# Kernel tuning notes

Hardware: AMD Instinct MI355X
Metric: run time of the kernel (lower is better)

## Reference

```python
import jax, jax.numpy as jnp
import numpy as np

B, S, D, F, E = 8, 2048, 768, 3072, 8


def setup_inputs() -> dict:
    key = jax.random.key(0)
    k1, k2, k3, k4 = jax.random.split(key, 4)
    return {
        "hidden_states": jax.random.normal(k1, (B, S, D), dtype=jnp.float32),
        "router_w": jax.random.normal(k2, (D, E), dtype=jnp.float32) * 0.02,
        "w_in": jax.random.normal(k3, (E, D, F), dtype=jnp.float32) * 0.02,
        "w_out": jax.random.normal(k4, (E, F, D), dtype=jnp.float32) * 0.02,
    }


def reference(hidden_states, router_w, w_in, w_out):
    b, s, d = hidden_states.shape
    x = hidden_states.reshape(-1, d)                    # [T, D] tokens
    router_logits = x @ router_w                        # [T, E]
    router_probs_full = jax.nn.softmax(router_logits, axis=-1)
    expert_index = jnp.argmax(router_probs_full, axis=-1)          # top-1 routing
    onehot = jax.nn.one_hot(expert_index, E, dtype=x.dtype)        # [T, E] router_mask
    top_prob = jnp.max(router_probs_full, axis=-1, keepdims=True)  # [T, 1] router_probs

    # Per-expert FFN (relu MLP); every token is processed by exactly one expert,
    # expert outputs overwrite the token (gather/scatter combine in the original).
    y = jnp.zeros_like(x)
    for e in range(E):  # fixed small expert count; weights structurally distinct
        h = jax.nn.relu(x @ w_in[e]) @ w_out[e]
        y = y + onehot[:, e:e + 1] * h

    out = (top_prob * y).reshape(b, s, d)
    return out, router_logits, expert_index
```

## Files before the change

kernel.cpp:

```cpp
#include <hip/hip_runtime.h>
#include <hip/hip_bf16.h>

constexpr int T  = 16384;
constexpr int Dh = 768;
constexpr int Fh = 3072;
constexpr int Eh = 8;
constexpr int MAXT2 = T / 256 + Eh;

typedef unsigned short ushort_t;
typedef __attribute__((ext_vector_type(8))) short  bf16x8;
typedef __attribute__((ext_vector_type(4))) float  f32x4;

static __device__ __forceinline__ ushort_t f2bf(float f) {
    unsigned u = __builtin_bit_cast(unsigned, f);
    u += 0x7FFFu + ((u >> 16) & 1u);
    return (ushort_t)(u >> 16);
}

__global__ void init_counts(int* counts) {
    if (threadIdx.x < Eh) counts[threadIdx.x] = 0;
}

__global__ __launch_bounds__(1024) void router_kernel(
    const float* __restrict__ x, const float* __restrict__ rw,
    float* __restrict__ logits_out, float* __restrict__ eidx_out,
    float* __restrict__ topp, int* __restrict__ counts, int* __restrict__ perm) {

    __shared__ float rwT[Eh][Dh];
    __shared__ int   sAmax[16];
    __shared__ int   sBase[Eh];

    int tid = threadIdx.x;
    for (int i = tid; i < Dh * Eh; i += 1024) {
        int d = i >> 3, e = i & 7;
        rwT[e][d] = rw[i];
    }
    __syncthreads();

    int wave = tid >> 6, lane = tid & 63;
    int t = blockIdx.x * 16 + wave;
    const float* xr = x + (size_t)t * Dh;

    double acc[Eh];
#pragma unroll
    for (int e = 0; e < Eh; ++e) acc[e] = 0.0;

#pragma unroll
    for (int j = 0; j < Dh / 256; ++j) {
        int d = lane * 4 + j * 256;
        const float4 xv = *(const float4*)(xr + d);
#pragma unroll
        for (int e = 0; e < Eh; ++e) {
            const float4 w = *(const float4*)&rwT[e][d];
            acc[e] += (double)xv.x * (double)w.x + (double)xv.y * (double)w.y
                    + (double)xv.z * (double)w.z + (double)xv.w * (double)w.w;
        }
    }
#pragma unroll
    for (int off = 32; off > 0; off >>= 1) {
#pragma unroll
        for (int e = 0; e < Eh; ++e) acc[e] += __shfl_xor(acc[e], off, 64);
    }

    int amax = 0;
    if (lane == 0) {
        float l32[Eh];
        float m = -3.4e38f;
#pragma unroll
        for (int e = 0; e < Eh; ++e) l32[e] = (float)acc[e];
#pragma unroll
        for (int e = 0; e < Eh; ++e) {
            if (l32[e] > m) { m = l32[e]; amax = e; }
        }
        float s = 0.f;
#pragma unroll
        for (int e = 0; e < Eh; ++e) s += expf(l32[e] - m);
#pragma unroll
        for (int e = 0; e < Eh; ++e) logits_out[(size_t)t * Eh + e] = l32[e];
        eidx_out[t] = (float)amax;
        topp[t]     = 1.0f / s;
        sAmax[wave] = amax;
    }
    __syncthreads();

    if (tid < Eh) {
        int c = 0;
#pragma unroll
        for (int w = 0; w < 16; ++w) c += (sAmax[w] == tid);
        sBase[tid] = (c > 0) ? atomicAdd(&counts[tid], c) : 0;
    }
    __syncthreads();

    if (lane == 0) {
        int prior = 0;
        for (int w = 0; w < wave; ++w) prior += (sAmax[w] == amax);
        perm[amax * T + sBase[amax] + prior] = t;
    }
}

__global__ void scan_counts(const int* counts, int* offsets,
                            int* tE, int* tGoff, int* tSlot0, int* tRows, int* nT) {
    if (threadIdx.x == 0) {
        int off = 0, n = 0;
        for (int e = 0; e < Eh; ++e) {
            offsets[e] = off;
            int c = counts[e];
            for (int t0 = 0; t0 < c; t0 += 256) {
                tE[n] = e; tGoff[n] = off + t0; tSlot0[n] = t0;
                tRows[n] = (c - t0 < 256) ? (c - t0) : 256;
                ++n;
            }
            off += c;
        }
        offsets[Eh] = off;
        nT[0] = n;
    }
}

__global__ void gather_cast_x(const float* __restrict__ x, const int* __restrict__ offsets,
                              const int* __restrict__ perm, ushort_t* __restrict__ Xg) {
    __shared__ int soff[Eh + 1];
    if (threadIdx.x < Eh + 1) soff[threadIdx.x] = offsets[threadIdx.x];
    __syncthreads();
    int q  = blockIdx.x * 256 + threadIdx.x;
    int g  = q / (Dh / 4);
    int cq = (q - g * (Dh / 4)) * 4;
    int e = 0;
#pragma unroll
    for (int i = 1; i < Eh; ++i) e += (g >= soff[i]);
    int tok = perm[e * T + (g - soff[e])];
    const float4 v = *(const float4*)(x + (size_t)tok * Dh + cq);
    ushort4 o;
    o.x = f2bf(v.x); o.y = f2bf(v.y); o.z = f2bf(v.z); o.w = f2bf(v.w);
    *(ushort4*)(Xg + (size_t)g * Dh + cq) = o;
}

__global__ void transpose_cvt(const float* __restrict__ src, ushort_t* __restrict__ dst,
                              int R, int C) {
    __shared__ ushort_t tile[32][33];
    int tx = threadIdx.x, ty = threadIdx.y;
    size_t base = (size_t)blockIdx.z * (size_t)R * (size_t)C;
    int c0 = blockIdx.x * 32, r0 = blockIdx.y * 32;
#pragma unroll
    for (int j = 0; j < 4; ++j) {
        int r = ty + j * 8;
        tile[r][tx] = f2bf(src[base + (size_t)(r0 + r) * C + c0 + tx]);
    }
    __syncthreads();
    int idx = ty * 32 + tx;
#pragma unroll
    for (int j = 0; j < 2; ++j) {
        int lin = idx + j * 256;
        int c  = lin >> 4;
        int rp = (lin & 15) * 2;
        ushort2 o = { tile[rp][c], tile[rp + 1][c] };
        *(ushort2*)(dst + base + (size_t)(c0 + c) * R + r0 + rp) = o;
    }
}

template<int KTOT, int NTOT, int MODE>
__global__ __launch_bounds__(512, 2) void moe_gemm2(
    const ushort_t* __restrict__ Aall, const ushort_t* __restrict__ Ball,
    const int* __restrict__ tE, const int* __restrict__ tGoff,
    const int* __restrict__ tSlot0, const int* __restrict__ tRows,
    const int* __restrict__ nT,
    const int* __restrict__ perm, const float* __restrict__ topp,
    void* __restrict__ Cout)
{
    int i = blockIdx.x;
    if (i >= nT[0]) return;
    int e     = tE[i];
    int goff  = tGoff[i];
    int slot0 = tSlot0[i];
    int rows  = tRows[i];
    int n0    = blockIdx.y * 256;

    const ushort_t* Ap = Aall + (size_t)goff * KTOT;
    const ushort_t* Bp = Ball + (size_t)e * KTOT * NTOT + (size_t)n0 * KTOT;

    __shared__ ushort_t As[2][256 * 64];
    __shared__ ushort_t Bs[2][256 * 64];
    __shared__ int   tokLds[256];
    __shared__ float probLds[256];

    int tid = threadIdx.x, lane = tid & 63, wid = tid >> 6;
    int wr2 = wid >> 2, wc2 = wid & 3;
    int gq  = lane >> 4, lm = lane & 15, l7 = lane & 7;

    if (MODE == 1 && tid < 256) {
        int tok = (tid < rows) ? perm[e * T + slot0 + tid] : 0;
        tokLds[tid]  = tok;
        probLds[tid] = (tid < rows) ? topp[tok] : 0.f;
    }

    f32x4 acc[4][4][2];
    const f32x4 zero = {0.f, 0.f, 0.f, 0.f};
#pragma unroll
    for (int q = 0; q < 4; ++q)
#pragma unroll
        for (int mi = 0; mi < 4; ++mi)
#pragma unroll
            for (int ni = 0; ni < 2; ++ni) acc[q][mi][ni] = zero;

    bf16x8 af[2][4];
    bf16x8 bb[2][2];

#define STAGE_A(BUF, HALF, KT) { \
    _Pragma("unroll") \
    for (int j = 0; j < 2; ++j) { \
        int c_ = tid + j * 512; \
        int rr = c_ >> 3, gg = c_ & 7; \
        int row_ = (HALF) * 128 + rr; \
        int srow_ = row_ < rows ? row_ : rows - 1; \
        const ushort_t* src_ = Ap + (size_t)srow_ * KTOT + (size_t)(KT) * 64 + ((gg ^ (rr & 7)) << 3); \
        __builtin_amdgcn_global_load_lds( \
            (const __attribute__((address_space(1))) unsigned int*)src_, \
            (__attribute__((address_space(3))) unsigned int*)&As[BUF][(size_t)row_ * 64 + gg * 8], 16, 0, 0); \
    } }

#define STAGE_B(BUF, HALF, KT) { \
    _Pragma("unroll") \
    for (int j = 0; j < 2; ++j) { \
        int c_ = tid + j * 512; \
        int rr = c_ >> 3, gg = c_ & 7; \
        int row_ = (HALF) * 128 + rr; \
        const ushort_t* src_ = Bp + (size_t)row_ * KTOT + (size_t)(KT) * 64 + ((gg ^ (rr & 7)) << 3); \
        __builtin_amdgcn_global_load_lds( \
            (const __attribute__((address_space(1))) unsigned int*)src_, \
            (__attribute__((address_space(3))) unsigned int*)&Bs[BUF][(size_t)row_ * 64 + gg * 8], 16, 0, 0); \
    } }

#define READ_FRAGS(TB, AH, BH) { \
    _Pragma("unroll") \
    for (int ks = 0; ks < 2; ++ks) { \
        const int cs_ = (((ks << 2) + gq) ^ l7) << 3; \
        _Pragma("unroll") \
        for (int mi = 0; mi < 4; ++mi) \
            af[ks][mi] = *(const bf16x8*)&As[TB][((AH) * 128 + wr2 * 64 + mi * 16 + lm) * 64 + cs_]; \
        _Pragma("unroll") \
        for (int ni = 0; ni < 2; ++ni) \
            bb[ks][ni] = *(const bf16x8*)&Bs[TB][((BH) * 128 + wc2 * 32 + ni * 16 + lm) * 64 + cs_]; \
    } }

#define MFMA_Q(Q) { \
    __builtin_amdgcn_s_setprio(1); \
    _Pragma("unroll") \
    for (int ks = 0; ks < 2; ++ks) \
        _Pragma("unroll") \
        for (int mi = 0; mi < 4; ++mi) \
            _Pragma("unroll") \
            for (int ni = 0; ni < 2; ++ni) \
                acc[Q][mi][ni] = __builtin_amdgcn_mfma_f32_16x16x32_bf16( \
                    af[ks][mi], bb[ks][ni], acc[Q][mi][ni], 0, 0, 0); \
    __builtin_amdgcn_s_setprio(0); }

    const int nkt = KTOT / 64;

    STAGE_A(0, 0, 0);
    STAGE_A(0, 1, 0);
    STAGE_B(0, 0, 0);
    STAGE_B(0, 1, 0);
    if (nkt > 1) {
        STAGE_B(1, 0, 1);
        STAGE_A(1, 0, 1);
        asm volatile("s_waitcnt vmcnt(4)" ::: "memory");
    } else {
        asm volatile("s_waitcnt vmcnt(0)" ::: "memory");
    }
    __builtin_amdgcn_sched_barrier(0);
    __builtin_amdgcn_s_barrier();

    for (int t = 0; t < nkt; ++t) {
        const int TB = t & 1;

        READ_FRAGS(TB, 0, 0);
        if (t + 1 < nkt) {
            STAGE_A(TB ^ 1, 1, t + 1);
            STAGE_B(TB ^ 1, 1, t + 1);
        }
        __builtin_amdgcn_s_barrier();
        MFMA_Q(0);
        __builtin_amdgcn_s_barrier();

        READ_FRAGS(TB, 1, 0);
        __builtin_amdgcn_s_barrier();
        MFMA_Q(1);
        __builtin_amdgcn_s_barrier();

        READ_FRAGS(TB, 0, 1);
        if (t + 2 < nkt) STAGE_B(TB, 0, t + 2);
        __builtin_amdgcn_s_barrier();
        MFMA_Q(2);
        __builtin_amdgcn_s_barrier();

        READ_FRAGS(TB, 1, 1);
        if (t + 2 < nkt) {
            STAGE_A(TB, 0, t + 2);
            asm volatile("s_waitcnt vmcnt(4)" ::: "memory");
        } else {
            asm volatile("s_waitcnt vmcnt(0)" ::: "memory");
        }
        __builtin_amdgcn_sched_barrier(0);
        __builtin_amdgcn_s_barrier();
        MFMA_Q(3);
        __builtin_amdgcn_s_barrier();
    }

    int cr = (lane >> 4) * 4;
    int cc = lane & 15;
#pragma unroll
    for (int q = 0; q < 4; ++q) {
        const int ah = q & 1, bh = q >> 1;
#pragma unroll
        for (int mi = 0; mi < 4; ++mi) {
#pragma unroll
            for (int r = 0; r < 4; ++r) {
                int m = ah * 128 + wr2 * 64 + mi * 16 + cr + r;
                if (m < rows) {
                    if (MODE == 0) {
                        ushort_t* hp = (ushort_t*)Cout + (size_t)(goff + m) * NTOT
                                     + n0 + bh * 128 + wc2 * 32 + cc;
#pragma unroll
                        for (int ni = 0; ni < 2; ++ni) {
                            float v = acc[q][mi][ni][r];
                            hp[ni * 16] = f2bf(v > 0.f ? v : 0.f);
                        }
                    } else {
                        int tok = tokLds[m];
                        float p = probLds[m];
                        float* op = (float*)Cout + (size_t)tok * NTOT
                                  + n0 + bh * 128 + wc2 * 32 + cc;
#pragma unroll
                        for (int ni = 0; ni < 2; ++ni) op[ni * 16] = acc[q][mi][ni][r] * p;
                    }
                }
            }
        }
    }
#undef STAGE_A
#undef STAGE_B
#undef READ_FRAGS
#undef MFMA_Q
}

constexpr size_t OFF_COUNTS  = 0;
constexpr size_t OFF_OFFSETS = 256;
constexpr size_t OFF_TILES   = 512;
constexpr size_t OFF_TOPP    = OFF_TILES + 4 * 144 * 5 + 64;
constexpr size_t OFF_PERM    = OFF_TOPP + (size_t)T * 4;
constexpr size_t OFF_XG      = (OFF_PERM + (size_t)Eh * T * 4 + 255) & ~(size_t)255;
constexpr size_t OFF_H       = (OFF_XG + (size_t)(T + 128) * Dh * 2 + 255) & ~(size_t)255;
constexpr size_t OFF_WIN     = (OFF_H + (size_t)(T + 128) * Fh * 2 + 255) & ~(size_t)255;
constexpr size_t OFF_WOUT    = (OFF_WIN + (size_t)Eh * Dh * Fh * 2 + 255) & ~(size_t)255;

extern "C" void kernel_launch(void* const* d_in, const int* in_sizes, int n_in,
                              void* d_out, int out_size, void* d_ws, size_t ws_size,
                              hipStream_t stream) {
    const float* x    = (const float*)d_in[0];
    const float* rw   = (const float*)d_in[1];
    const float* w_in = (const float*)d_in[2];
    const float* w_out= (const float*)d_in[3];

    float* out    = (float*)d_out;
    float* logits = out + (size_t)T * Dh;
    float* eidx   = logits + (size_t)T * Eh;

    char* ws = (char*)d_ws;
    int*      counts  = (int*)(ws + OFF_COUNTS);
    int*      offsets = (int*)(ws + OFF_OFFSETS);
    int*      tE      = (int*)(ws + OFF_TILES);
    int*      tGoff   = tE + 144;
    int*      tSlot0  = tGoff + 144;
    int*      tRows   = tSlot0 + 144;
    int*      nT      = tRows + 144;
    float*    topp    = (float*)(ws + OFF_TOPP);
    int*      perm    = (int*)(ws + OFF_PERM);
    ushort_t* Xg      = (ushort_t*)(ws + OFF_XG);
    ushort_t* h       = (ushort_t*)(ws + OFF_H);
    ushort_t* WinT    = (ushort_t*)(ws + OFF_WIN);
    ushort_t* WoutT   = (ushort_t*)(ws + OFF_WOUT);

    init_counts<<<1, 64, 0, stream>>>(counts);
    router_kernel<<<T / 16, 1024, 0, stream>>>(x, rw, logits, eidx, topp, counts, perm);
    scan_counts<<<1, 64, 0, stream>>>(counts, offsets, tE, tGoff, tSlot0, tRows, nT);
    gather_cast_x<<<(T * (Dh / 4)) / 256, 256, 0, stream>>>(x, offsets, perm, Xg);
    transpose_cvt<<<dim3(Fh / 32, Dh / 32, Eh), dim3(32, 8), 0, stream>>>(w_in, WinT, Dh, Fh);
    transpose_cvt<<<dim3(Dh / 32, Fh / 32, Eh), dim3(32, 8), 0, stream>>>(w_out, WoutT, Fh, Dh);
    moe_gemm2<Dh, Fh, 0><<<dim3(MAXT2, Fh / 256), 512, 0, stream>>>(
        Xg, WinT, tE, tGoff, tSlot0, tRows, nT, perm, topp, (void*)h);
    moe_gemm2<Fh, Dh, 1><<<dim3(MAXT2, Dh / 256), 512, 0, stream>>>(
        h, WoutT, tE, tGoff, tSlot0, tRows, nT, perm, topp, (void*)out);
}
```

Measured before the change: 511.2 us.

## Restructure MoE GEMM warp tiling to 2x4 waves with 128x64 per-wave tiles

Changes the per-wave output tile in the grouped GEMM from four 64x32 quadrants to one 128x64 block, so B fragments are read once per k-tile and only A fragments are re-read in four phases. The stage schedule now loads full A and B tiles instead of half tiles, with its own waitcnt placement. The aim is less LDS fragment traffic and fewer split stages per k-step, at the cost of a new waitcnt/barrier pipeline that may hide load latency less well. It also parallelises the tile-list scan across 8 lanes and replaces the counts-init kernel with hipMemsetAsync.

```diff
diff --git a/kernel.cpp b/kernel.cpp
--- a/kernel.cpp
+++ b/kernel.cpp
@@ -17,10 +17,6 @@
     return (ushort_t)(u >> 16);
 }
 
-__global__ void init_counts(int* counts) {
-    if (threadIdx.x < Eh) counts[threadIdx.x] = 0;
-}
-
 __global__ __launch_bounds__(1024) void router_kernel(
     const float* __restrict__ x, const float* __restrict__ rw,
     float* __restrict__ logits_out, float* __restrict__ eidx_out,
@@ -100,20 +96,29 @@
 
 __global__ void scan_counts(const int* counts, int* offsets,
                             int* tE, int* tGoff, int* tSlot0, int* tRows, int* nT) {
-    if (threadIdx.x == 0) {
-        int off = 0, n = 0;
-        for (int e = 0; e < Eh; ++e) {
-            offsets[e] = off;
-            int c = counts[e];
-            for (int t0 = 0; t0 < c; t0 += 256) {
-                tE[n] = e; tGoff[n] = off + t0; tSlot0[n] = t0;
-                tRows[n] = (c - t0 < 256) ? (c - t0) : 256;
-                ++n;
-            }
-            off += c;
-        }
-        offsets[Eh] = off;
-        nT[0] = n;
+    int lane = threadIdx.x;
+    if (lane < Eh) {
+        int coff = 0, toff = 0;
+        for (int e = 0; e < lane; ++e) {
+            int ce = counts[e];
+            coff += ce;
+            toff += (ce + 255) >> 8;
+        }
+        int c = counts[lane];
+        offsets[lane] = coff;
+        int myt = (c + 255) >> 8;
+        for (int k = 0; k < myt; ++k) {
+            int idx = toff + k;
+            tE[idx]     = lane;
+            tGoff[idx]  = coff + k * 256;
+            tSlot0[idx] = k * 256;
+            int rem = c - k * 256;
+            tRows[idx]  = rem < 256 ? rem : 256;
+        }
+        if (lane == Eh - 1) {
+            offsets[Eh] = coff + c;
+            nT[0] = toff + myt;
+        }
     }
 }
 
@@ -184,8 +189,8 @@
     __shared__ float probLds[256];
 
     int tid = threadIdx.x, lane = tid & 63, wid = tid >> 6;
-    int wr2 = wid >> 2, wc2 = wid & 3;
-    int gq  = lane >> 4, lm = lane & 15, l7 = lane & 7;
+    int wr = wid >> 2, wc = wid & 3;
+    int gq = lane >> 4, lm = lane & 15, l7 = lane & 7;
 
     if (MODE == 1 && tid < 256) {
         int tok = (tid < rows) ? perm[e * T + slot0 + tid] : 0;
@@ -193,76 +198,75 @@
         probLds[tid] = (tid < rows) ? topp[tok] : 0.f;
     }
 
-    f32x4 acc[4][4][2];
+    f32x4 acc[8][4];
     const f32x4 zero = {0.f, 0.f, 0.f, 0.f};
 #pragma unroll
-    for (int q = 0; q < 4; ++q)
-#pragma unroll
-        for (int mi = 0; mi < 4; ++mi)
-#pragma unroll
-            for (int ni = 0; ni < 2; ++ni) acc[q][mi][ni] = zero;
-
-    bf16x8 af[2][4];
-    bf16x8 bb[2][2];
-
-#define STAGE_A(BUF, HALF, KT) { \
-    _Pragma("unroll") \
-    for (int j = 0; j < 2; ++j) { \
+    for (int mi = 0; mi < 8; ++mi)
+#pragma unroll
+        for (int ni = 0; ni < 4; ++ni) acc[mi][ni] = zero;
+
+    bf16x8 af[2][2];
+    bf16x8 bb[2][4];
+
+#define STAGE_A(BUF, KT) { \
+    _Pragma("unroll") \
+    for (int j = 0; j < 4; ++j) { \
         int c_ = tid + j * 512; \
         int rr = c_ >> 3, gg = c_ & 7; \
-        int row_ = (HALF) * 128 + rr; \
-        int srow_ = row_ < rows ? row_ : rows - 1; \
+        int srow_ = rr < rows ? rr : rows - 1; \
         const ushort_t* src_ = Ap + (size_t)srow_ * KTOT + (size_t)(KT) * 64 + ((gg ^ (rr & 7)) << 3); \
         __builtin_amdgcn_global_load_lds( \
             (const __attribute__((address_space(1))) unsigned int*)src_, \
-            (__attribute__((address_space(3))) unsigned int*)&As[BUF][(size_t)row_ * 64 + gg * 8], 16, 0, 0); \
+            (__attribute__((address_space(3))) unsigned int*)&As[BUF][rr * 64 + gg * 8], 16, 0, 0); \
     } }
 
-#define STAGE_B(BUF, HALF, KT) { \
-    _Pragma("unroll") \
-    for (int j = 0; j < 2; ++j) { \
+#define STAGE_B(BUF, KT) { \
+    _Pragma("unroll") \
+    for (int j = 0; j < 4; ++j) { \
         int c_ = tid + j * 512; \
         int rr = c_ >> 3, gg = c_ & 7; \
-        int row_ = (HALF) * 128 + rr; \
-        const ushort_t* src_ = Bp + (size_t)row_ * KTOT + (size_t)(KT) * 64 + ((gg ^ (rr & 7)) << 3); \
+        const ushort_t* src_ = Bp + (size_t)rr * KTOT + (size_t)(KT) * 64 + ((gg ^ (rr & 7)) << 3); \
         __builtin_amdgcn_global_load_lds( \
             (const __attribute__((address_space(1))) unsigned int*)src_, \
-            (__attribute__((address_space(3))) unsigned int*)&Bs[BUF][(size_t)row_ * 64 + gg * 8], 16, 0, 0); \
+            (__attribute__((address_space(3))) unsigned int*)&Bs[BUF][rr * 64 + gg * 8], 16, 0, 0); \
     } }
 
-#define READ_FRAGS(TB, AH, BH) { \
-    _Pragma("unroll") \
-    for (int ks = 0; ks < 2; ++ks) { \
-        const int cs_ = (((ks << 2) + gq) ^ l7) << 3; \
-        _Pragma("unroll") \
-        for (int mi = 0; mi < 4; ++mi) \
-            af[ks][mi] = *(const bf16x8*)&As[TB][((AH) * 128 + wr2 * 64 + mi * 16 + lm) * 64 + cs_]; \
-        _Pragma("unroll") \
-        for (int ni = 0; ni < 2; ++ni) \
-            bb[ks][ni] = *(const bf16x8*)&Bs[TB][((BH) * 128 + wc2 * 32 + ni * 16 + lm) * 64 + cs_]; \
-    } }
-
-#define MFMA_Q(Q) { \
-    __builtin_amdgcn_s_setprio(1); \
+#define READ_A(TB, P) { \
     _Pragma("unroll") \
     for (int ks = 0; ks < 2; ++ks) \
         _Pragma("unroll") \
-        for (int mi = 0; mi < 4; ++mi) \
+        for (int j = 0; j < 2; ++j) \
+            af[ks][j] = *(const bf16x8*)&As[TB][ \
+                (wr * 128 + ((P) * 2 + j) * 16 + lm) * 64 + ((((ks << 2) + gq) ^ l7) << 3)]; \
+    }
+
+#define READ_B(TB) { \
+    _Pragma("unroll") \
+    for (int ks = 0; ks < 2; ++ks) \
+        _Pragma("unroll") \
+        for (int ni = 0; ni < 4; ++ni) \
+            bb[ks][ni] = *(const bf16x8*)&Bs[TB][ \
+                (wc * 64 + ni * 16 + lm) * 64 + ((((ks << 2) + gq) ^ l7) << 3)]; \
+    }
+
+#define MFMA_P(P) { \
+    __builtin_amdgcn_s_setprio(1); \
+    _Pragma("unroll") \
+    for (int ks = 0; ks < 2; ++ks) \
+        _Pragma("unroll") \
+        for (int j = 0; j < 2; ++j) \
             _Pragma("unroll") \
-            for (int ni = 0; ni < 2; ++ni) \
-                acc[Q][mi][ni] = __builtin_amdgcn_mfma_f32_16x16x32_bf16( \
-                    af[ks][mi], bb[ks][ni], acc[Q][mi][ni], 0, 0, 0); \
+            for (int ni = 0; ni < 4; ++ni) \
+                acc[(P) * 2 + j][ni] = __builtin_amdgcn_mfma_f32_16x16x32_bf16( \
+                    af[ks][j], bb[ks][ni], acc[(P) * 2 + j][ni], 0, 0, 0); \
     __builtin_amdgcn_s_setprio(0); }
 
     const int nkt = KTOT / 64;
 
-    STAGE_A(0, 0, 0);
-    STAGE_A(0, 1, 0);
-    STAGE_B(0, 0, 0);
-    STAGE_B(0, 1, 0);
+    STAGE_A(0, 0);
+    STAGE_B(0, 0);
     if (nkt > 1) {
-        STAGE_B(1, 0, 1);
-        STAGE_A(1, 0, 1);
+        STAGE_B(1, 1);
         asm volatile("s_waitcnt vmcnt(4)" ::: "memory");
     } else {
         asm volatile("s_waitcnt vmcnt(0)" ::: "memory");
@@ -273,74 +277,69 @@
     for (int t = 0; t < nkt; ++t) {
         const int TB = t & 1;
 
-        READ_FRAGS(TB, 0, 0);
-        if (t + 1 < nkt) {
-            STAGE_A(TB ^ 1, 1, t + 1);
-            STAGE_B(TB ^ 1, 1, t + 1);
-        }
-        __builtin_amdgcn_s_barrier();
-        MFMA_Q(0);
-        __builtin_amdgcn_s_barrier();
-
-        READ_FRAGS(TB, 1, 0);
-        __builtin_amdgcn_s_barrier();
-        MFMA_Q(1);
-        __builtin_amdgcn_s_barrier();
-
-        READ_FRAGS(TB, 0, 1);
-        if (t + 2 < nkt) STAGE_B(TB, 0, t + 2);
-        __builtin_amdgcn_s_barrier();
-        MFMA_Q(2);
-        __builtin_amdgcn_s_barrier();
-
-        READ_FRAGS(TB, 1, 1);
+        READ_B(TB);
+        READ_A(TB, 0);
+        if (t + 1 < nkt) STAGE_A(TB ^ 1, t + 1);
+        __builtin_amdgcn_s_barrier();
+        MFMA_P(0);
+        __builtin_amdgcn_s_barrier();
+
+        READ_A(TB, 1);
+        if (t + 2 < nkt) STAGE_B(TB, t + 2);
+        __builtin_amdgcn_s_barrier();
+        MFMA_P(1);
+        __builtin_amdgcn_s_barrier();
+
+        READ_A(TB, 2);
+        __builtin_amdgcn_s_barrier();
+        MFMA_P(2);
+        __builtin_amdgcn_s_barrier();
+
+        READ_A(TB, 3);
         if (t + 2 < nkt) {
-            STAGE_A(TB, 0, t + 2);
             asm volatile("s_waitcnt vmcnt(4)" ::: "memory");
-        } else {
+            __builtin_amdgcn_sched_barrier(0);
+        } else if (t + 1 < nkt) {
             asm volatile("s_waitcnt vmcnt(0)" ::: "memory");
-        }
-        __builtin_amdgcn_sched_barrier(0);
-        __builtin_amdgcn_s_barrier();
-        MFMA_Q(3);
+            __builtin_amdgcn_sched_barrier(0);
+        }
+        __builtin_amdgcn_s_barrier();
+        MFMA_P(3);
         __builtin_amdgcn_s_barrier();
     }
 
     int cr = (lane >> 4) * 4;
     int cc = lane & 15;
 #pragma unroll
-    for (int q = 0; q < 4; ++q) {
-        const int ah = q & 1, bh = q >> 1;
-#pragma unroll
-        for (int mi = 0; mi < 4; ++mi) {
-#pragma unroll
-            for (int r = 0; r < 4; ++r) {
-                int m = ah * 128 + wr2 * 64 + mi * 16 + cr + r;
-                if (m < rows) {
-                    if (MODE == 0) {
-                        ushort_t* hp = (ushort_t*)Cout + (size_t)(goff + m) * NTOT
-                                     + n0 + bh * 128 + wc2 * 32 + cc;
-#pragma unroll
-                        for (int ni = 0; ni < 2; ++ni) {
-                            float v = acc[q][mi][ni][r];
-                            hp[ni * 16] = f2bf(v > 0.f ? v : 0.f);
-                        }
-                    } else {
-                        int tok = tokLds[m];
-                        float p = probLds[m];
-                        float* op = (float*)Cout + (size_t)tok * NTOT
-                                  + n0 + bh * 128 + wc2 * 32 + cc;
-#pragma unroll
-                        for (int ni = 0; ni < 2; ++ni) op[ni * 16] = acc[q][mi][ni][r] * p;
+    for (int mi = 0; mi < 8; ++mi) {
+#pragma unroll
+        for (int r = 0; r < 4; ++r) {
+            int m = wr * 128 + mi * 16 + cr + r;
+            if (m < rows) {
+                if (MODE == 0) {
+                    ushort_t* hp = (ushort_t*)Cout + (size_t)(goff + m) * NTOT
+                                 + n0 + wc * 64 + cc;
+#pragma unroll
+                    for (int ni = 0; ni < 4; ++ni) {
+                        float v = acc[mi][ni][r];
+                        hp[ni * 16] = f2bf(v > 0.f ? v : 0.f);
                     }
+                } else {
+                    int tok = tokLds[m];
+                    float p = probLds[m];
+                    float* op = (float*)Cout + (size_t)tok * NTOT
+                              + n0 + wc * 64 + cc;
+#pragma unroll
+                    for (int ni = 0; ni < 4; ++ni) op[ni * 16] = acc[mi][ni][r] * p;
                 }
             }
         }
     }
 #undef STAGE_A
 #undef STAGE_B
-#undef READ_FRAGS
-#undef MFMA_Q
+#undef READ_A
+#undef READ_B
+#undef MFMA_P
 }
 
 constexpr size_t OFF_COUNTS  = 0;
@@ -380,7 +379,7 @@
     ushort_t* WinT    = (ushort_t*)(ws + OFF_WIN);
     ushort_t* WoutT   = (ushort_t*)(ws + OFF_WOUT);
 
-    init_counts<<<1, 64, 0, stream>>>(counts);
+    hipMemsetAsync(counts, 0, Eh * sizeof(int), stream);
     router_kernel<<<T / 16, 1024, 0, stream>>>(x, rw, logits, eidx, topp, counts, perm);
     scan_counts<<<1, 64, 0, stream>>>(counts, offsets, tE, tGoff, tSlot0, tRows, nT);
     gather_cast_x<<<(T * (Dh / 4)) / 256, 256, 0, stream>>>(x, offsets, perm, Xg);
```

Measured after the change: 518.1 us. About the same (+1.4%).
